# Performance work log

Hardware: AMD Instinct MI355X
Metric: run time of the kernel (lower is better)

## Reference

```python
import jax, jax.numpy as jnp
import numpy as np

DIM = 128
HEADS = 32
DIM_HEAD = 64
INNER = DIM * DIM_HEAD  # 8192, as written in the source (dim * dim_head)
D = INNER // HEADS      # 256 per-head dim
B, N = 1, 2048
ROT = 64                # partial rotary width (l)
SCALE = DIM ** (-0.5)   # source uses dim**-0.5, not head-dim


def _rotate_half(x):
    # x: [..., l]; split as (j d) with j=2 -> cat(-x2, x1)
    x1, x2 = jnp.split(x, 2, axis=-1)
    return jnp.concatenate((-x2, x1), axis=-1)


def _apply_rotary(q, k, freqs):
    # freqs: [n, l]; q,k: [b,h,n,d] with l <= d (partial rotary)
    l = freqs.shape[-1]
    cos, sin = jnp.cos(freqs), jnp.sin(freqs)  # broadcast over b,h
    ql, qr = q[..., :l], q[..., l:]
    kl, kr = k[..., :l], k[..., l:]
    ql = ql * cos + _rotate_half(ql) * sin
    kl = kl * cos + _rotate_half(kl) * sin
    return jnp.concatenate((ql, qr), axis=-1), jnp.concatenate((kl, kr), axis=-1)


def setup_inputs() -> dict:
    key = jax.random.key(0)
    k1, k2, k3, k4, k5 = jax.random.split(key, 5)
    return {
        "x": jax.random.normal(k1, (B, N, DIM), dtype=jnp.float32),
        "Wqkv": jax.random.normal(k2, (3 * INNER, DIM), dtype=jnp.float32) * 0.02,
        "Wproj": jax.random.normal(k3, (DIM, INNER), dtype=jnp.float32) * 0.02,
        "bproj": jax.random.normal(k4, (DIM,), dtype=jnp.float32) * 0.02,
        "rotary_pos_emb": jax.random.normal(k5, (N, ROT), dtype=jnp.float32),
    }


def reference(x, Wqkv, Wproj, bproj, rotary_pos_emb):
    b, n, _ = x.shape
    qkv = x @ Wqkv.T                                   # [b, n, 3*inner]
    qkv = qkv.reshape(b, n, 3, HEADS, D)               # (qkv h d) ordering
    qkv = jnp.transpose(qkv, (2, 0, 3, 1, 4))          # [3, b, h, n, d]
    q, k, v = qkv[0], qkv[1], qkv[2]
    q, k = _apply_rotary(q, k, rotary_pos_emb)
    energy = jnp.einsum("bhid,bhjd->bhij", q, k) * SCALE  # [b,h,n,n]
    attn = jax.nn.softmax(energy, axis=-1)
    out = jnp.einsum("bhij,bhjd->bhid", attn, v)       # [b,h,n,d]
    out = jnp.transpose(out, (0, 2, 1, 3)).reshape(b, n, INNER)
    return out @ Wproj.T + bproj
```

## Files before the change

### kernel.cpp

```cpp
#include <hip/hip_runtime.h>


typedef unsigned short u16;
typedef unsigned int u32;
typedef __attribute__((ext_vector_type(8))) u16 u16x8;
typedef __attribute__((ext_vector_type(8))) __bf16 bf16x8;
typedef __attribute__((ext_vector_type(4))) float f32x4;
typedef __attribute__((ext_vector_type(4))) u32 u32x4;
typedef __attribute__((ext_vector_type(2))) u32 u32x2;

#define DEV static __device__ __forceinline__

DEV u16 f2b(float f) {
  __bf16 h = (__bf16)f;
  return __builtin_bit_cast(u16, h);
}
DEV float b2f(u16 b) {
  u32 u = ((u32)b) << 16;
  return __builtin_bit_cast(float, u);
}
DEV u32 pk2(float a, float b) { return (u32)f2b(a) | ((u32)f2b(b) << 16); }

DEV f32x4 mfma16(u16x8 a, u16x8 b, f32x4 c) {
  return __builtin_amdgcn_mfma_f32_16x16x32_bf16(
      __builtin_bit_cast(bf16x8, a), __builtin_bit_cast(bf16x8, b), c, 0, 0, 0);
}

DEV int swz(int row, int kelem, int rowBytes) {
  return row * rowBytes + ((kelem * 2) ^ ((row & 7) << 4));
}

DEV void dma16(const void* g, void* l) {
  __builtin_amdgcn_global_load_lds(
      (const __attribute__((address_space(1))) void*)g,
      (__attribute__((address_space(3))) void*)l, 16, 0, 0);
}

__global__ __launch_bounds__(256) void k_cvt(const float* __restrict__ src,
                                             u16* __restrict__ dst, int n8) {
  int i = blockIdx.x * 256 + threadIdx.x;
  if (i >= n8) return;
  const float4* s = (const float4*)src;
  float4 a = s[i * 2], b = s[i * 2 + 1];
  u16x8 o;
  o[0] = f2b(a.x); o[1] = f2b(a.y); o[2] = f2b(a.z); o[3] = f2b(a.w);
  o[4] = f2b(b.x); o[5] = f2b(b.y); o[6] = f2b(b.z); o[7] = f2b(b.w);
  *(u16x8*)(dst + (size_t)i * 8) = o;
}

__global__ __launch_bounds__(256) void k_qkv(const u16* __restrict__ xb,
                                             const u16* __restrict__ wb,
                                             u16* __restrict__ qw,
                                             u16* __restrict__ kw,
                                             u16* __restrict__ vw) {
  __shared__ char lds[65536];
  const int tid = threadIdx.x;
  const int rt = blockIdx.x % 192, nt = blockIdx.x / 192;
  const int r0 = rt * 128, n0 = nt * 128;
#pragma unroll
  for (int p = 0; p < 8; ++p) {
    int row = p * 16 + (tid >> 4);
    int k0 = (tid & 15) * 8;
    *(u16x8*)(lds + swz(row, k0, 256)) =
        *(const u16x8*)(wb + (size_t)(r0 + row) * 128 + k0);
    *(u16x8*)(lds + 32768 + swz(row, k0, 256)) =
        *(const u16x8*)(xb + (size_t)(n0 + row) * 128 + k0);
  }
  __syncthreads();
  const int wid = tid >> 6, lane = tid & 63, lq = lane & 15, g = lane >> 4;
  const int wr = wid >> 1, wn = wid & 1;
  const bool isV = (r0 >= 16384);
  f32x4 acc[4][4] = {};
#pragma unroll
  for (int ks = 0; ks < 4; ++ks) {
    u16x8 wa[4], xa[4];
#pragma unroll
    for (int i = 0; i < 4; ++i) {
      int rw = wr * 64 + i * 16 + lq;
      wa[i] = *(const u16x8*)(lds + swz(rw, ks * 32 + g * 8, 256));
      int rx = wn * 64 + i * 16 + lq;
      xa[i] = *(const u16x8*)(lds + 32768 + swz(rx, ks * 32 + g * 8, 256));
    }
    if (!isV) {
#pragma unroll
      for (int i = 0; i < 4; ++i)
#pragma unroll
        for (int j = 0; j < 4; ++j) acc[i][j] = mfma16(wa[i], xa[j], acc[i][j]);
    } else {
#pragma unroll
      for (int i = 0; i < 4; ++i)
#pragma unroll
        for (int j = 0; j < 4; ++j) acc[i][j] = mfma16(xa[j], wa[i], acc[i][j]);
    }
  }
  const float SMQ = 0.08838834764831845f * 1.4426950408889634f;
  if (!isV) {
#pragma unroll
    for (int i = 0; i < 4; ++i) {
      int rb = r0 + wr * 64 + i * 16 + g * 4;
      u16* dst0 = (rb >= 8192) ? kw : qw;
      float scl = (rb >= 8192) ? 1.0f : SMQ;
      int hd = rb & 8191;
      int h = hd >> 8, db = hd & 255;
#pragma unroll
      for (int j = 0; j < 4; ++j) {
        int n = n0 + wn * 64 + j * 16 + lq;
        u32x2 pk;
        pk.x = pk2(acc[i][j][0] * scl, acc[i][j][1] * scl);
        pk.y = pk2(acc[i][j][2] * scl, acc[i][j][3] * scl);
        *(u32x2*)(dst0 + ((size_t)h * 2048 + n) * 256 + db) = pk;
      }
    }
  } else {
#pragma unroll
    for (int i = 0; i < 4; ++i) {
      int rc = r0 - 16384 + wr * 64 + i * 16 + lq;
      int h = rc >> 8, d = rc & 255;
#pragma unroll
      for (int j = 0; j < 4; ++j) {
        int nb = n0 + wn * 64 + j * 16 + g * 4;
        u32x2 pk;
        pk.x = pk2(acc[i][j][0], acc[i][j][1]);
        pk.y = pk2(acc[i][j][2], acc[i][j][3]);
        *(u32x2*)(vw + ((size_t)h * 256 + d) * 2048 + nb) = pk;
      }
    }
  }
}

__global__ __launch_bounds__(256) void k_rope(u16* __restrict__ qw,
                                              u16* __restrict__ kw,
                                              const float* __restrict__ fr) {
  int idx = blockIdx.x * 256 + threadIdx.x;
  int seg = idx & 3;
  int n = (idx >> 2) & 2047;
  int h = (idx >> 13) & 31;
  u16* base = ((idx >> 18) ? kw : qw) + ((size_t)h * 2048 + n) * 256 + seg * 8;
  u16x8 lo = *(const u16x8*)base;
  u16x8 hi = *(const u16x8*)(base + 32);
  const float* f = fr + n * 64 + seg * 8;
  u16x8 nlo, nhi;
#pragma unroll
  for (int e = 0; e < 8; ++e) {
    float fl = f[e], fh = f[e + 32];
    float sl, cl, sh, ch;
    __sincosf(fl, &sl, &cl);
    __sincosf(fh, &sh, &ch);
    float a = b2f(lo[e]), b = b2f(hi[e]);
    nlo[e] = f2b(a * cl - b * sl);
    nhi[e] = f2b(b * ch + a * sh);
  }
  *(u16x8*)base = nlo;
  *(u16x8*)(base + 32) = nhi;
}

__global__ __launch_bounds__(256, 2) void k_attn(const u16* __restrict__ qw,
                                                 const u16* __restrict__ kw,
                                                 const u16* __restrict__ vw,
                                                 u16* __restrict__ ow) {
  __shared__ char lds[65536];
  const int tid = threadIdx.x;
  const int h = blockIdx.x & 31;
  const int qb = blockIdx.x >> 5;
  const int wid = tid >> 6, lane = tid & 63, lq = lane & 15, g = lane >> 4;
  const int q0 = qb * 128 + wid * 32;
  const int lane16 = lane * 16;

  const u16* kbase = kw + (size_t)h * 2048 * 256;
  const u16* vbase = vw + (size_t)h * 256 * 2048;

  int koff[4], voff[4];
#pragma unroll
  for (int i = 0; i < 4; ++i) {
    int s = wid * 4 + i;
    koff[i] = ((s >> 3) * 16 + lq) * 256 + (s & 7) * 32 + g * 8;
    voff[i] = (s * 16 + lq) * 2048 + g * 8;
  }

  u16x8 qf[2][8];
  {
    const u16* q0p = qw + ((size_t)h * 2048 + q0 + lq) * 256;
#pragma unroll
    for (int ds = 0; ds < 8; ++ds) {
      qf[0][ds] = *(const u16x8*)(q0p + ds * 32 + g * 8);
      qf[1][ds] = *(const u16x8*)(q0p + 16 * 256 + ds * 32 + g * 8);
    }
  }

  f32x4 oacc[2][16] = {};
  float mrun[2] = {-1e30f, -1e30f}, lrun[2] = {0.f, 0.f};

#define STAGE(T)                                                     \
  {                                                                  \
    const int kv0 = (T) * 32;                                        \
    char* kb_ = lds + ((T) & 1) * 32768;                             \
    _Pragma("unroll") for (int i = 0; i < 4; ++i) {                  \
      dma16(kbase + (size_t)kv0 * 256 + koff[i],                     \
            kb_ + (wid * 4 + i) * 1024);                             \
      dma16(vbase + kv0 + voff[i],                                   \
            kb_ + 16384 + (wid * 4 + i) * 1024);                     \
    }                                                                \
  }

  STAGE(0);

  for (int t = 0; t < 64; ++t) {
    if (t < 63) {
      STAGE(t + 1);
      asm volatile("s_waitcnt vmcnt(8)" ::: "memory");
    } else {
      asm volatile("s_waitcnt vmcnt(0)" ::: "memory");
    }
    __builtin_amdgcn_s_barrier();
    asm volatile("" ::: "memory");

    const char* kb = lds + (t & 1) * 32768;

    f32x4 sa[2][2] = {};
    __builtin_amdgcn_s_setprio(1);
#pragma unroll
    for (int ds = 0; ds < 8; ++ds) {
#pragma unroll
      for (int f = 0; f < 2; ++f) {
        u16x8 ka = *(const u16x8*)(kb + lane16 + (f * 8 + ds) * 1024);
        sa[0][f] = mfma16(ka, qf[0][ds], sa[0][f]);
        sa[1][f] = mfma16(ka, qf[1][ds], sa[1][f]);
      }
    }
    __builtin_amdgcn_s_setprio(0);

    u32 pk[2][2][2];
#pragma unroll
    for (int c = 0; c < 2; ++c) {
      float mt = -1e30f;
#pragma unroll
      for (int f = 0; f < 2; ++f)
#pragma unroll
        for (int r = 0; r < 4; ++r) mt = fmaxf(mt, sa[c][f][r]);
      mt = fmaxf(mt, __shfl_xor(mt, 16));
      mt = fmaxf(mt, __shfl_xor(mt, 32));
      bool skip = __all(mt - mrun[c] <= 8.0f);
      if (!skip) {
        float mnew = fmaxf(mrun[c], mt);
        float corr = exp2f(mrun[c] - mnew);
        lrun[c] *= corr;
#pragma unroll
        for (int di = 0; di < 16; ++di) {
          oacc[c][di][0] *= corr; oacc[c][di][1] *= corr;
          oacc[c][di][2] *= corr; oacc[c][di][3] *= corr;
        }
        mrun[c] = mnew;
      }
      float lt = 0.f;
#pragma unroll
      for (int f = 0; f < 2; ++f) {
        float p0 = exp2f(sa[c][f][0] - mrun[c]);
        float p1 = exp2f(sa[c][f][1] - mrun[c]);
        float p2 = exp2f(sa[c][f][2] - mrun[c]);
        float p3 = exp2f(sa[c][f][3] - mrun[c]);
        lt += (p0 + p1) + (p2 + p3);
        pk[c][f][0] = pk2(p0, p1);
        pk[c][f][1] = pk2(p2, p3);
      }
      lt += __shfl_xor(lt, 16);
      lt += __shfl_xor(lt, 32);
      lrun[c] += lt;
    }

    u16x8 pb[2];
#pragma unroll
    for (int c = 0; c < 2; ++c) {
      u32x4 bu;
#pragma unroll
      for (int tt = 0; tt < 4; ++tt) {
        int src = (2 * (g & 1) + (tt >> 1)) * 16 + lq;
        u32 vlo = (u32)__shfl((int)pk[c][0][tt & 1], src);
        u32 vhi = (u32)__shfl((int)pk[c][1][tt & 1], src);
        bu[tt] = (g < 2) ? vlo : vhi;
      }
      pb[c] = __builtin_bit_cast(u16x8, bu);
    }

    __builtin_amdgcn_s_setprio(1);
#pragma unroll
    for (int di = 0; di < 16; ++di) {
      u16x8 va = *(const u16x8*)(kb + 16384 + lane16 + di * 1024);
      oacc[0][di] = mfma16(va, pb[0], oacc[0][di]);
      oacc[1][di] = mfma16(va, pb[1], oacc[1][di]);
    }
    __builtin_amdgcn_s_setprio(0);

    __builtin_amdgcn_s_barrier();
    asm volatile("" ::: "memory");
  }
#undef STAGE

#pragma unroll
  for (int c = 0; c < 2; ++c) {
    float inv = 1.0f / lrun[c];
    u16* orow = ow + (size_t)(q0 + c * 16 + lq) * 8192 + h * 256;
#pragma unroll
    for (int di = 0; di < 16; ++di) {
      u32x2 o2;
      o2.x = pk2(oacc[c][di][0] * inv, oacc[c][di][1] * inv);
      o2.y = pk2(oacc[c][di][2] * inv, oacc[c][di][3] * inv);
      *(u32x2*)(orow + di * 16 + g * 4) = o2;
    }
  }
}

__global__ __launch_bounds__(256) void k_proj(const u16* __restrict__ ow,
                                              const u16* __restrict__ wp,
                                              float* __restrict__ part) {
  __shared__ char lds[49152];
  const int tid = threadIdx.x;
  const int nt = blockIdx.x >> 3, kc = blockIdx.x & 7;
  const int n0 = nt * 64, kb = kc * 1024;
  const int wid = tid >> 6, lane = tid & 63, lq = lane & 15, g = lane >> 4;
  f32x4 acc[8] = {};
  for (int kt = 0; kt < 8; ++kt) {
    int kk = kb + kt * 128;
#pragma unroll
    for (int p = 0; p < 4; ++p) {
      int nr = p * 16 + (tid >> 4);
      int k0 = (tid & 15) * 8;
      *(u16x8*)(lds + swz(nr, k0, 256)) =
          *(const u16x8*)(ow + (size_t)(n0 + nr) * 8192 + kk + k0);
    }
#pragma unroll
    for (int p = 0; p < 8; ++p) {
      int er = p * 16 + (tid >> 4);
      int k0 = (tid & 15) * 8;
      *(u16x8*)(lds + 16384 + swz(er, k0, 256)) =
          *(const u16x8*)(wp + (size_t)er * 8192 + kk + k0);
    }
    __syncthreads();
#pragma unroll
    for (int ks = 0; ks < 4; ++ks) {
      int nr = wid * 16 + lq;
      u16x8 oa = *(const u16x8*)(lds + swz(nr, ks * 32 + g * 8, 256));
#pragma unroll
      for (int ef = 0; ef < 8; ++ef) {
        int er = ef * 16 + lq;
        u16x8 wf = *(const u16x8*)(lds + 16384 + swz(er, ks * 32 + g * 8, 256));
        acc[ef] = mfma16(oa, wf, acc[ef]);
      }
    }
    __syncthreads();
  }
  float* pb = part + (size_t)kc * 262144;
#pragma unroll
  for (int ef = 0; ef < 8; ++ef)
#pragma unroll
    for (int r = 0; r < 4; ++r) {
      int n = n0 + wid * 16 + g * 4 + r;
      pb[n * 128 + ef * 16 + lq] = acc[ef][r];
    }
}

__global__ __launch_bounds__(256) void k_reduce(const float* __restrict__ part,
                                                const float* __restrict__ bias,
                                                float* __restrict__ out) {
  int i = blockIdx.x * 256 + threadIdx.x;
  float s = bias[i & 127];
#pragma unroll
  for (int c = 0; c < 8; ++c) s += part[(size_t)c * 262144 + i];
  out[i] = s;
}

extern "C" void kernel_launch(void* const* d_in, const int* in_sizes, int n_in,
                              void* d_out, int out_size, void* d_ws, size_t ws_size,
                              hipStream_t stream) {
  const float* x = (const float*)d_in[0];
  const float* wqkv = (const float*)d_in[1];
  const float* wproj = (const float*)d_in[2];
  const float* bproj = (const float*)d_in[3];
  const float* rope = (const float*)d_in[4];
  char* ws = (char*)d_ws;
  u16* xb    = (u16*)(ws);
  u16* wqkvb = (u16*)(ws + 524288);
  u16* wpb   = (u16*)(ws + 6815744);
  u16* qw    = (u16*)(ws + 8912896);
  u16* kw    = (u16*)(ws + 42467328);
  u16* vw    = (u16*)(ws + 76021760);
  u16* owv   = (u16*)(ws + 109576192);
  float* part = (float*)(ws + 8912896);

  k_cvt<<<128, 256, 0, stream>>>(x, xb, 32768);
  k_cvt<<<1536, 256, 0, stream>>>(wqkv, wqkvb, 393216);
  k_cvt<<<512, 256, 0, stream>>>(wproj, wpb, 131072);
  k_qkv<<<3072, 256, 0, stream>>>(xb, wqkvb, qw, kw, vw);
  k_rope<<<2048, 256, 0, stream>>>(qw, kw, rope);
  k_attn<<<512, 256, 0, stream>>>(qw, kw, vw, owv);
  k_proj<<<256, 256, 0, stream>>>(owv, wpb, part);
  k_reduce<<<1024, 256, 0, stream>>>(part, bproj, (float*)d_out);
}
```

Before: 246.8 us.

## Rewrite attention kernel with 32x32 MFMA, 512-thread blocks and triple-buffered KV

The attention kernel moves from 16x16x32 MFMA tiles to 32x32x16 tiles, so each wave handles 32 query rows as a single accumulator group. Blocks grow to 512 threads covering 256 queries, with half the waves loading K and half loading V. A triple-buffered LDS ring with a two-tile prefetch distance replaces double buffering and drops the trailing barrier. The aims are fewer LDS reads per MFMA, fewer shuffles in softmax, and better load/compute overlap. The costs are 96KB of LDS per block, which limits occupancy, and fewer blocks in the grid (256).

```diff
diff --git a/kernel.cpp b/kernel.cpp
--- a/kernel.cpp
+++ b/kernel.cpp
@@ -6,6 +6,7 @@
 typedef __attribute__((ext_vector_type(8))) u16 u16x8;
 typedef __attribute__((ext_vector_type(8))) __bf16 bf16x8;
 typedef __attribute__((ext_vector_type(4))) float f32x4;
+typedef __attribute__((ext_vector_type(16))) float f32x16;
 typedef __attribute__((ext_vector_type(4))) u32 u32x4;
 typedef __attribute__((ext_vector_type(2))) u32 u32x2;
 
@@ -23,6 +24,10 @@
 
 DEV f32x4 mfma16(u16x8 a, u16x8 b, f32x4 c) {
   return __builtin_amdgcn_mfma_f32_16x16x32_bf16(
+      __builtin_bit_cast(bf16x8, a), __builtin_bit_cast(bf16x8, b), c, 0, 0, 0);
+}
+DEV f32x16 mfma32(u16x8 a, u16x8 b, f32x16 c) {
+  return __builtin_amdgcn_mfma_f32_32x32x16_bf16(
       __builtin_bit_cast(bf16x8, a), __builtin_bit_cast(bf16x8, b), c, 0, 0, 0);
 }
 
@@ -154,159 +159,157 @@
   *(u16x8*)(base + 32) = nhi;
 }
 
-__global__ __launch_bounds__(256, 2) void k_attn(const u16* __restrict__ qw,
+__global__ __launch_bounds__(512, 2) void k_attn(const u16* __restrict__ qw,
                                                  const u16* __restrict__ kw,
                                                  const u16* __restrict__ vw,
                                                  u16* __restrict__ ow) {
-  __shared__ char lds[65536];
+  __shared__ char lds[98304];
   const int tid = threadIdx.x;
   const int h = blockIdx.x & 31;
   const int qb = blockIdx.x >> 5;
-  const int wid = tid >> 6, lane = tid & 63, lq = lane & 15, g = lane >> 4;
-  const int q0 = qb * 128 + wid * 32;
+  const int wid = tid >> 6, lane = tid & 63;
+  const int l31 = lane & 31, h2 = lane >> 5;
+  const int q0w = qb * 256 + wid * 32;
   const int lane16 = lane * 16;
 
   const u16* kbase = kw + (size_t)h * 2048 * 256;
   const u16* vbase = vw + (size_t)h * 256 * 2048;
 
-  int koff[4], voff[4];
+  const bool isK = (wid < 4);
+  const int dstslot = isK ? wid * 4 : 16 + (wid - 4) * 4;
+  int off[4];
 #pragma unroll
   for (int i = 0; i < 4; ++i) {
-    int s = wid * 4 + i;
-    koff[i] = ((s >> 3) * 16 + lq) * 256 + (s & 7) * 32 + g * 8;
-    voff[i] = (s * 16 + lq) * 2048 + g * 8;
-  }
-
-  u16x8 qf[2][8];
+    if (isK) {
+      int s = wid * 4 + i;
+      off[i] = l31 * 256 + s * 16 + h2 * 8;
+    } else {
+      int u = (wid - 4) * 4 + i;
+      off[i] = ((u >> 1) * 32 + l31) * 2048 + (u & 1) * 16 + h2 * 8;
+    }
+  }
+
+  u16x8 qf[16];
   {
-    const u16* q0p = qw + ((size_t)h * 2048 + q0 + lq) * 256;
-#pragma unroll
-    for (int ds = 0; ds < 8; ++ds) {
-      qf[0][ds] = *(const u16x8*)(q0p + ds * 32 + g * 8);
-      qf[1][ds] = *(const u16x8*)(q0p + 16 * 256 + ds * 32 + g * 8);
-    }
-  }
-
-  f32x4 oacc[2][16] = {};
-  float mrun[2] = {-1e30f, -1e30f}, lrun[2] = {0.f, 0.f};
-
-#define STAGE(T)                                                     \
-  {                                                                  \
-    const int kv0 = (T) * 32;                                        \
-    char* kb_ = lds + ((T) & 1) * 32768;                             \
-    _Pragma("unroll") for (int i = 0; i < 4; ++i) {                  \
-      dma16(kbase + (size_t)kv0 * 256 + koff[i],                     \
-            kb_ + (wid * 4 + i) * 1024);                             \
-      dma16(vbase + kv0 + voff[i],                                   \
-            kb_ + 16384 + (wid * 4 + i) * 1024);                     \
-    }                                                                \
-  }
-
-  STAGE(0);
+    const u16* qp = qw + ((size_t)h * 2048 + q0w + l31) * 256 + h2 * 8;
+#pragma unroll
+    for (int dt = 0; dt < 16; ++dt) qf[dt] = *(const u16x8*)(qp + dt * 16);
+  }
+
+  f32x16 oacc[8] = {};
+  float mrun = -1e30f, lrun = 0.f;
+
+#define STAGE(T, BUF)                                               \
+  {                                                                 \
+    const int kv0_ = (T) * 32;                                      \
+    char* b_ = lds + (BUF) * 32768;                                 \
+    if (isK) {                                                      \
+      _Pragma("unroll") for (int i = 0; i < 4; ++i)                 \
+          dma16(kbase + (size_t)kv0_ * 256 + off[i],                \
+                b_ + (dstslot + i) * 1024);                         \
+    } else {                                                        \
+      _Pragma("unroll") for (int i = 0; i < 4; ++i)                 \
+          dma16(vbase + kv0_ + off[i], b_ + (dstslot + i) * 1024);  \
+    }                                                               \
+  }
+
+  STAGE(0, 0);
+  STAGE(1, 1);
+  int rb = 0, sb = 2;
 
   for (int t = 0; t < 64; ++t) {
-    if (t < 63) {
-      STAGE(t + 1);
-      asm volatile("s_waitcnt vmcnt(8)" ::: "memory");
-    } else {
+    if (t < 63)
+      asm volatile("s_waitcnt vmcnt(4)" ::: "memory");
+    else
       asm volatile("s_waitcnt vmcnt(0)" ::: "memory");
-    }
     __builtin_amdgcn_s_barrier();
     asm volatile("" ::: "memory");
-
-    const char* kb = lds + (t & 1) * 32768;
-
-    f32x4 sa[2][2] = {};
+    if (t < 62) STAGE(t + 2, sb);
+
+    const char* kb = lds + rb * 32768;
+
+    f32x16 sa = {};
     __builtin_amdgcn_s_setprio(1);
 #pragma unroll
-    for (int ds = 0; ds < 8; ++ds) {
-#pragma unroll
-      for (int f = 0; f < 2; ++f) {
-        u16x8 ka = *(const u16x8*)(kb + lane16 + (f * 8 + ds) * 1024);
-        sa[0][f] = mfma16(ka, qf[0][ds], sa[0][f]);
-        sa[1][f] = mfma16(ka, qf[1][ds], sa[1][f]);
-      }
+    for (int dt = 0; dt < 16; ++dt) {
+      u16x8 ka = *(const u16x8*)(kb + dt * 1024 + lane16);
+      sa = mfma32(ka, qf[dt], sa);
     }
     __builtin_amdgcn_s_setprio(0);
 
-    u32 pk[2][2][2];
-#pragma unroll
-    for (int c = 0; c < 2; ++c) {
-      float mt = -1e30f;
-#pragma unroll
-      for (int f = 0; f < 2; ++f)
-#pragma unroll
-        for (int r = 0; r < 4; ++r) mt = fmaxf(mt, sa[c][f][r]);
-      mt = fmaxf(mt, __shfl_xor(mt, 16));
-      mt = fmaxf(mt, __shfl_xor(mt, 32));
-      bool skip = __all(mt - mrun[c] <= 8.0f);
-      if (!skip) {
-        float mnew = fmaxf(mrun[c], mt);
-        float corr = exp2f(mrun[c] - mnew);
-        lrun[c] *= corr;
-#pragma unroll
-        for (int di = 0; di < 16; ++di) {
-          oacc[c][di][0] *= corr; oacc[c][di][1] *= corr;
-          oacc[c][di][2] *= corr; oacc[c][di][3] *= corr;
-        }
-        mrun[c] = mnew;
-      }
-      float lt = 0.f;
-#pragma unroll
-      for (int f = 0; f < 2; ++f) {
-        float p0 = exp2f(sa[c][f][0] - mrun[c]);
-        float p1 = exp2f(sa[c][f][1] - mrun[c]);
-        float p2 = exp2f(sa[c][f][2] - mrun[c]);
-        float p3 = exp2f(sa[c][f][3] - mrun[c]);
-        lt += (p0 + p1) + (p2 + p3);
-        pk[c][f][0] = pk2(p0, p1);
-        pk[c][f][1] = pk2(p2, p3);
-      }
-      lt += __shfl_xor(lt, 16);
-      lt += __shfl_xor(lt, 32);
-      lrun[c] += lt;
-    }
-
-    u16x8 pb[2];
-#pragma unroll
-    for (int c = 0; c < 2; ++c) {
-      u32x4 bu;
-#pragma unroll
-      for (int tt = 0; tt < 4; ++tt) {
-        int src = (2 * (g & 1) + (tt >> 1)) * 16 + lq;
-        u32 vlo = (u32)__shfl((int)pk[c][0][tt & 1], src);
-        u32 vhi = (u32)__shfl((int)pk[c][1][tt & 1], src);
-        bu[tt] = (g < 2) ? vlo : vhi;
-      }
-      pb[c] = __builtin_bit_cast(u16x8, bu);
-    }
+    float m8[8];
+#pragma unroll
+    for (int r = 0; r < 8; ++r) m8[r] = fmaxf(sa[r], sa[r + 8]);
+#pragma unroll
+    for (int r = 0; r < 4; ++r) m8[r] = fmaxf(m8[r], m8[r + 4]);
+    float mt = fmaxf(fmaxf(m8[0], m8[1]), fmaxf(m8[2], m8[3]));
+    mt = fmaxf(mt, __shfl_xor(mt, 32));
+    if (!__all(mt - mrun <= 8.0f)) {
+      float mnew = fmaxf(mrun, mt);
+      float corr = __builtin_amdgcn_exp2f(mrun - mnew);
+      lrun *= corr;
+#pragma unroll
+      for (int dt = 0; dt < 8; ++dt)
+#pragma unroll
+        for (int r = 0; r < 16; ++r) oacc[dt][r] *= corr;
+      mrun = mnew;
+    }
+    float p[16];
+#pragma unroll
+    for (int r = 0; r < 16; ++r)
+      p[r] = __builtin_amdgcn_exp2f(sa[r] - mrun);
+    float s8[8];
+#pragma unroll
+    for (int r = 0; r < 8; ++r) s8[r] = p[r] + p[r + 8];
+#pragma unroll
+    for (int r = 0; r < 4; ++r) s8[r] = s8[r] + s8[r + 4];
+    float lt = (s8[0] + s8[1]) + (s8[2] + s8[3]);
+    lt += __shfl_xor(lt, 32);
+    lrun += lt;
+
+    u32 pkk[8], xpk[8];
+#pragma unroll
+    for (int j = 0; j < 8; ++j) pkk[j] = pk2(p[2 * j], p[2 * j + 1]);
+#pragma unroll
+    for (int j = 0; j < 8; ++j) xpk[j] = (u32)__shfl_xor((int)pkk[j], 32);
+    u32x4 b0v, b1v;
+    b0v[0] = h2 ? xpk[2] : pkk[0];
+    b0v[1] = h2 ? xpk[3] : pkk[1];
+    b0v[2] = h2 ? pkk[2] : xpk[0];
+    b0v[3] = h2 ? pkk[3] : xpk[1];
+    b1v[0] = h2 ? xpk[6] : pkk[4];
+    b1v[1] = h2 ? xpk[7] : pkk[5];
+    b1v[2] = h2 ? pkk[6] : xpk[4];
+    b1v[3] = h2 ? pkk[7] : xpk[5];
+    u16x8 pb0 = __builtin_bit_cast(u16x8, b0v);
+    u16x8 pb1 = __builtin_bit_cast(u16x8, b1v);
 
     __builtin_amdgcn_s_setprio(1);
 #pragma unroll
-    for (int di = 0; di < 16; ++di) {
-      u16x8 va = *(const u16x8*)(kb + 16384 + lane16 + di * 1024);
-      oacc[0][di] = mfma16(va, pb[0], oacc[0][di]);
-      oacc[1][di] = mfma16(va, pb[1], oacc[1][di]);
+    for (int dt = 0; dt < 8; ++dt) {
+      u16x8 v0 = *(const u16x8*)(kb + 16384 + (dt * 2) * 1024 + lane16);
+      oacc[dt] = mfma32(v0, pb0, oacc[dt]);
+      u16x8 v1 = *(const u16x8*)(kb + 16384 + (dt * 2 + 1) * 1024 + lane16);
+      oacc[dt] = mfma32(v1, pb1, oacc[dt]);
     }
     __builtin_amdgcn_s_setprio(0);
 
-    __builtin_amdgcn_s_barrier();
-    asm volatile("" ::: "memory");
+    rb = (rb == 2) ? 0 : rb + 1;
+    sb = (sb == 2) ? 0 : sb + 1;
   }
 #undef STAGE
 
-#pragma unroll
-  for (int c = 0; c < 2; ++c) {
-    float inv = 1.0f / lrun[c];
-    u16* orow = ow + (size_t)(q0 + c * 16 + lq) * 8192 + h * 256;
-#pragma unroll
-    for (int di = 0; di < 16; ++di) {
+  float inv = 1.0f / lrun;
+  u16* orow = ow + (size_t)(q0w + l31) * 8192 + h * 256 + h2 * 4;
+#pragma unroll
+  for (int dt = 0; dt < 8; ++dt)
+#pragma unroll
+    for (int k = 0; k < 4; ++k) {
       u32x2 o2;
-      o2.x = pk2(oacc[c][di][0] * inv, oacc[c][di][1] * inv);
-      o2.y = pk2(oacc[c][di][2] * inv, oacc[c][di][3] * inv);
-      *(u32x2*)(orow + di * 16 + g * 4) = o2;
-    }
-  }
+      o2.x = pk2(oacc[dt][4 * k] * inv, oacc[dt][4 * k + 1] * inv);
+      o2.y = pk2(oacc[dt][4 * k + 2] * inv, oacc[dt][4 * k + 3] * inv);
+      *(u32x2*)(orow + dt * 32 + k * 8) = o2;
+    }
 }
 
 __global__ __launch_bounds__(256) void k_proj(const u16* __restrict__ ow,
@@ -391,7 +394,7 @@
   k_cvt<<<512, 256, 0, stream>>>(wproj, wpb, 131072);
   k_qkv<<<3072, 256, 0, stream>>>(xb, wqkvb, qw, kw, vw);
   k_rope<<<2048, 256, 0, stream>>>(qw, kw, rope);
-  k_attn<<<512, 256, 0, stream>>>(qw, kw, vw, owv);
+  k_attn<<<256, 512, 0, stream>>>(qw, kw, vw, owv);
   k_proj<<<256, 256, 0, stream>>>(owv, wpb, part);
   k_reduce<<<1024, 256, 0, stream>>>(part, bproj, (float*)d_out);
 }
```

Result: faster. 229.4 us (-7.1%).
